# Performance work log

Hardware: AMD Instinct MI355X
Metric: run time of the kernel (lower is better)

The kernel has to match this reference:

```python
import jax, jax.numpy as jnp
import numpy as np

NPOINT = 1024   # samples (farthest point sampling count)
RADIUS = 0.2    # ball query radius
K = 32          # neighbors per ball


def farthest_point_sample(xyz, npoint):
    # xyz: [B, N, 3] -> idx: [B, npoint] int32
    B, N, _ = xyz.shape
    def body(carry, _):
        dists, farthest = carry                      # [B,N], [B]
        centroid = jnp.take_along_axis(xyz, farthest[:, None, None], axis=1)  # [B,1,3]
        d = jnp.sum((xyz - centroid) ** 2, axis=-1)  # [B,N]
        dists = jnp.minimum(dists, d)
        nxt = jnp.argmax(dists, axis=-1).astype(jnp.int32)
        return (dists, nxt), farthest
    init = (jnp.full((B, N), 1e10, dtype=xyz.dtype), jnp.zeros((B,), jnp.int32))
    _, idx = jax.lax.scan(body, init, None, length=npoint)
    return jnp.transpose(idx)  # [B, npoint]


def query_ball_point(radius, k, xyz, new_xyz):
    # returns idx: [B, S, k] int32 -- first k in-radius point indices,
    # padded with the first found index (TF query_ball_point semantics)
    N = xyz.shape[1]
    sqd = jnp.sum((new_xyz[:, :, None, :] - xyz[:, None, :, :]) ** 2, axis=-1)  # [B,S,N]
    cand = jnp.where(sqd <= radius * radius, jnp.arange(N, dtype=jnp.int32)[None, None, :], N)
    idx = jnp.sort(cand, axis=-1)[..., :k]          # [B,S,k]
    first = idx[..., :1]
    return jnp.where(idx == N, first, idx).astype(jnp.int32)


def group_point(x, idx):
    # x: [B,N,C], idx: [B,S,k] -> [B,S,k,C]
    return jax.vmap(lambda xb, ib: xb[ib])(x, idx)


def setup_inputs() -> dict:
    key = jax.random.key(0)
    ks = jax.random.split(key, 8)
    B, N, C = 16, 4096, 64
    xyz = jax.random.uniform(ks[0], (B, N, 3), dtype=jnp.float32)
    points = jax.random.normal(ks[1], (B, N, C), dtype=jnp.float32)
    cin = 3 + C  # use_xyz concat
    widths = [64, 64, 128]
    W, b, c = [], [], cin
    for i, w in enumerate(widths):
        W.append(jax.random.normal(ks[2 + i], (c, w), dtype=jnp.float32) * (1.0 / np.sqrt(c)))
        b.append(jnp.zeros((w,), dtype=jnp.float32))
        c = w
    return {"xyz": xyz, "points": points,
            "W0": W[0], "b0": b[0], "W1": W[1], "b1": b[1], "W2": W[2], "b2": b[2]}


def reference(xyz, points, W0, b0, W1, b1, W2, b2):
    # --- sample_and_group ---
    fps_idx = farthest_point_sample(xyz, NPOINT)                 # [B,S]
    new_xyz = jax.vmap(lambda xb, ib: xb[ib])(xyz, fps_idx)      # [B,S,3]
    idx = query_ball_point(RADIUS, K, xyz, new_xyz)              # [B,S,K]
    grouped_xyz = group_point(xyz, idx) - new_xyz[:, :, None, :] # [B,S,K,3]
    grouped_points = group_point(points, idx)                    # [B,S,K,C]
    new_points = jnp.concatenate([grouped_xyz, grouped_points], axis=-1)  # [B,S,K,3+C]
    # --- shared 1x1-conv MLP (bn=False, relu) ---
    for W, bb in ((W0, b0), (W1, b1), (W2, b2)):
        new_points = jax.nn.relu(jnp.einsum('bskc,cd->bskd', new_points, W) + bb)
    # --- max pool over neighborhood ---
    new_points = jnp.max(new_points, axis=2)                     # [B,S,Cout]
    return new_xyz, new_points, idx
```

## Files before the change

### kernel.cpp

```cpp
#include <hip/hip_runtime.h>

#define BB 16
#define NN 4096
#define SS 1024
#define KNB 32
#define FPT 16
#define FNW 4

typedef unsigned long long ull;
typedef float v2f __attribute__((ext_vector_type(2)));

__device__ __forceinline__ float sqd3(float dx, float dy, float dz) {
    return __fadd_rn(__fadd_rn(__fmul_rn(dx, dx), __fmul_rn(dy, dy)), __fmul_rn(dz, dz));
}

#define DPPMAX(m, ctrl, rm)                                                              \
    {                                                                                    \
        unsigned _t = (unsigned)__builtin_amdgcn_update_dpp((int)(m), (int)(m), (ctrl),  \
                                                            (rm), 0xf, false);           \
        (m) = ((m) > _t) ? (m) : _t;                                                     \
    }

__global__ __launch_bounds__(256) void fused1_kernel(const float* __restrict__ xyz,
                                                     const float* __restrict__ points,
                                                     const float* __restrict__ W0,
                                                     const float* __restrict__ b0,
                                                     float* __restrict__ P1,
                                                     float4* __restrict__ xyz4,
                                                     float* __restrict__ out_newxyz) {
    __shared__ union {
        struct {
            float4 pts4[NN];
            ull    keys[2][FNW];
            int    hist[SS];
        } f;
        float w0s[67 * 64];
    } sm;

    const int t = threadIdx.x;

    if (blockIdx.x < BB) {
        const int b = blockIdx.x;
        const int lane = t & 63;
        const float* src = xyz + (size_t)b * (NN * 3) + (size_t)t * (FPT * 3);

        v2f px2[8], py2[8], pz2[8], d2[8];
        {
            float c48[48];
#pragma unroll
            for (int m = 0; m < 12; ++m) {
                float4 v = ((const float4*)src)[m];
                c48[4 * m + 0] = v.x; c48[4 * m + 1] = v.y;
                c48[4 * m + 2] = v.z; c48[4 * m + 3] = v.w;
            }
#pragma unroll
            for (int j = 0; j < 8; ++j) {
                px2[j] = (v2f){c48[6 * j + 0], c48[6 * j + 3]};
                py2[j] = (v2f){c48[6 * j + 1], c48[6 * j + 4]};
                pz2[j] = (v2f){c48[6 * j + 2], c48[6 * j + 5]};
                d2[j]  = (v2f){1e10f, 1e10f};
                sm.f.pts4[t * FPT + 2 * j + 0] = make_float4(px2[j].x, py2[j].x, pz2[j].x, 0.f);
                sm.f.pts4[t * FPT + 2 * j + 1] = make_float4(px2[j].y, py2[j].y, pz2[j].y, 0.f);
            }
        }
        __syncthreads();

        int far = 0;
        for (int it = 0; it < SS; ++it) {
            if (t == 0) sm.f.hist[it] = far;
            if (it == SS - 1) break;
            float4 c = sm.f.pts4[far];

            float bv0 = -1.f, bv1 = -1.f;
            int bn0 = 0, bn1 = 0;
            {
#pragma clang fp contract(off)
                v2f cx2 = {c.x, c.x}, cy2 = {c.y, c.y}, cz2 = {c.z, c.z};
#pragma unroll
                for (int j = 0; j < 4; ++j) {
                    v2f dx = px2[j] - cx2;
                    v2f dy = py2[j] - cy2;
                    v2f dz = pz2[j] - cz2;
                    v2f s = (dx * dx + dy * dy) + dz * dz;
                    float d0 = fminf(d2[j].x, s.x);
                    float d1 = fminf(d2[j].y, s.y);
                    d2[j] = (v2f){d0, d1};
                    bool g0 = d0 > bv0; bv0 = g0 ? d0 : bv0; bn0 = g0 ? (t * FPT + 2 * j + 0) : bn0;
                    bool g1 = d1 > bv0; bv0 = g1 ? d1 : bv0; bn0 = g1 ? (t * FPT + 2 * j + 1) : bn0;
                }
#pragma unroll
                for (int j = 4; j < 8; ++j) {
                    v2f dx = px2[j] - cx2;
                    v2f dy = py2[j] - cy2;
                    v2f dz = pz2[j] - cz2;
                    v2f s = (dx * dx + dy * dy) + dz * dz;
                    float d0 = fminf(d2[j].x, s.x);
                    float d1 = fminf(d2[j].y, s.y);
                    d2[j] = (v2f){d0, d1};
                    bool g0 = d0 > bv1; bv1 = g0 ? d0 : bv1; bn1 = g0 ? (t * FPT + 2 * j + 0) : bn1;
                    bool g1 = d1 > bv1; bv1 = g1 ? d1 : bv1; bn1 = g1 ? (t * FPT + 2 * j + 1) : bn1;
                }
            }
            bool gm = bv1 > bv0;
            float bv = gm ? bv1 : bv0;
            int bn = gm ? bn1 : bn0;

            unsigned mb = __float_as_uint(bv);
            DPPMAX(mb, 0x111, 0xf);
            DPPMAX(mb, 0x112, 0xf);
            DPPMAX(mb, 0x114, 0xf);
            DPPMAX(mb, 0x118, 0xf);
            DPPMAX(mb, 0x142, 0xa);
            DPPMAX(mb, 0x143, 0xc);
            unsigned vmb = (unsigned)__builtin_amdgcn_readlane((int)mb, 63);

            ull ball = __ballot(__float_as_uint(bv) == vmb);
            int sel = __ffsll(ball) - 1;
            int widx = __builtin_amdgcn_readlane(bn, sel);

            const int par = it & 1;
            if (lane == 0) {
                sm.f.keys[par][t >> 6] = ((ull)vmb << 32) | (unsigned)(~widx);
            }
            __syncthreads();
            ulonglong2 ka = *(const ulonglong2*)&sm.f.keys[par][0];
            ulonglong2 kb = *(const ulonglong2*)&sm.f.keys[par][2];
            ull a0 = (ka.x > ka.y) ? ka.x : ka.y;
            ull a1 = (kb.x > kb.y) ? kb.x : kb.y;
            ull best = (a0 > a1) ? a0 : a1;
            far = (int)(~(unsigned)best);
        }
        __syncthreads();
#pragma unroll
        for (int r = 0; r < 4; ++r) {
            int it2 = t + 256 * r;
            int fi = sm.f.hist[it2];
            float4 c = sm.f.pts4[fi];
            size_t o = ((size_t)b * SS + it2) * 3;
            out_newxyz[o + 0] = c.x;
            out_newxyz[o + 1] = c.y;
            out_newxyz[o + 2] = c.z;
        }
    } else {
        for (int i = t; i < 67 * 64; i += 256) sm.w0s[i] = W0[i];
        __syncthreads();
        const int lane = t & 63;
        const int wv = t >> 6;

        {
            int n0 = (blockIdx.x - BB) * 256 + t;
            xyz4[n0] = make_float4(xyz[3 * n0 + 0], xyz[3 * n0 + 1], xyz[3 * n0 + 2], 0.f);
        }

        const float bias = b0[lane];
        const int base = (blockIdx.x - BB) * 256 + wv * 64;
        for (int pi = 0; pi < 64; ++pi) {
            const int n = base + pi;
            const float* xp = xyz + (size_t)n * 3;
            const float* pp = points + (size_t)n * 64;
            float acc = bias;
            acc = fmaf(xp[0], sm.w0s[0 * 64 + lane], acc);
            acc = fmaf(xp[1], sm.w0s[1 * 64 + lane], acc);
            acc = fmaf(xp[2], sm.w0s[2 * 64 + lane], acc);
#pragma unroll 8
            for (int c = 0; c < 64; ++c) acc = fmaf(pp[c], sm.w0s[(3 + c) * 64 + lane], acc);
            P1[(size_t)n * 64 + lane] = acc;
        }
    }
}

__global__ __launch_bounds__(256, 2) void k3_kernel(const float4* __restrict__ xyz4,
                                                    const float* __restrict__ P1,
                                                    const float* __restrict__ W0,
                                                    const float* __restrict__ W1,
                                                    const float* __restrict__ b1,
                                                    const float* __restrict__ W2,
                                                    const float* __restrict__ b2,
                                                    float* __restrict__ d_out) {
    const int t = threadIdx.x;
    const int lane = t & 63;
    const int wv = t >> 6;
    const int b = blockIdx.x >> 10;

    __shared__ float w2t[128][68];
    __shared__ float hs[4][8][64];
    __shared__ float part[4][128];
    __shared__ int   ids[KNB];
    __shared__ int   bq[2][FNW];

    float* out_newxyz = d_out;
    float* out_points = d_out + (size_t)BB * SS * 3;
    float* out_idx    = d_out + (size_t)BB * SS * 3 + (size_t)BB * SS * 128;

    const size_t q = (size_t)blockIdx.x;
    const float nx = out_newxyz[q * 3 + 0];
    const float ny = out_newxyz[q * 3 + 1];
    const float nz = out_newxyz[q * 3 + 2];

#pragma unroll
    for (int r = 0; r < 8; ++r) {
        int m = t + 256 * r;
        int o = m & 127;
        int i4 = m >> 7;
        float4 v;
        v.x = W2[(4 * i4 + 0) * 128 + o];
        v.y = W2[(4 * i4 + 1) * 128 + o];
        v.z = W2[(4 * i4 + 2) * 128 + o];
        v.w = W2[(4 * i4 + 3) * 128 + o];
        *(float4*)&w2t[o][4 * i4] = v;
    }

    {
        const float4* xb4 = xyz4 + (size_t)b * NN;
        const float R2 = 0.04f;
        const ull ltm = (1ull << lane) - 1ull;
        int total = 0, c0 = 0, pr = 0;
        float4 pcA = xb4[t];
        float4 pcB = xb4[256 + t];
        while (true) {
            float4 curA = pcA, curB = pcB;
            int nc0 = c0 + 512;
            if (nc0 < NN) {
                pcA = xb4[nc0 + t];
                pcB = xb4[nc0 + 256 + t];
            }
            float dA = sqd3(curA.x - nx, curA.y - ny, curA.z - nz);
            float dB = sqd3(curB.x - nx, curB.y - ny, curB.z - nz);
            bool inA = (dA <= R2);
            bool inB = (dB <= R2);
            ull mA = __ballot(inA);
            ull mB = __ballot(inB);
            if (lane == 0) bq[pr][wv] = __popcll(mA) | (__popcll(mB) << 8);
            __syncthreads();
            int p0 = bq[pr][0], p1 = bq[pr][1], p2 = bq[pr][2], p3 = bq[pr][3];
            int a0 = p0 & 0xff, a1 = p1 & 0xff, a2 = p2 & 0xff, a3 = p3 & 0xff;
            int e0 = p0 >> 8, e1 = p1 >> 8, e2 = p2 >> 8, e3 = p3 >> 8;
            int sumA = a0 + a1 + a2 + a3;
            int baseA = total + (wv > 0 ? a0 : 0) + (wv > 1 ? a1 : 0) + (wv > 2 ? a2 : 0);
            int baseB = total + sumA + (wv > 0 ? e0 : 0) + (wv > 1 ? e1 : 0) + (wv > 2 ? e2 : 0);
            int posA = baseA + __popcll(mA & ltm);
            int posB = baseB + __popcll(mB & ltm);
            if (inA && posA < KNB) ids[posA] = c0 + t;
            if (inB && posB < KNB) ids[posB] = c0 + 256 + t;
            total += sumA + e0 + e1 + e2 + e3;
            c0 = nc0;
            pr ^= 1;
            if (total >= KNB || c0 >= NN) break;
        }
        __syncthreads();
        int cnt = (total < KNB) ? total : KNB;
        if (t >= cnt && t < KNB) ids[t] = ids[0];
    }
    __syncthreads();
    if (t < KNB) out_idx[q * KNB + t] = (float)ids[t];

    const float qv = nx * W0[lane] + ny * W0[64 + lane] + nz * W0[128 + lane];
    float w1col[64];
#pragma unroll
    for (int i = 0; i < 64; ++i) w1col[i] = W1[i * 64 + lane];
    const float b1v = b1[lane];

    const float* P1b = P1 + (size_t)b * NN * 64;
#pragma unroll
    for (int kk = 0; kk < 8; ++kk) {
        int n = ids[wv * 8 + kk];
        float v = P1b[(size_t)n * 64 + lane] - qv;
        hs[wv][kk][lane] = fmaxf(v, 0.f);
    }

    float acc[8];
#pragma unroll
    for (int kk = 0; kk < 8; ++kk) acc[kk] = b1v;
#pragma unroll
    for (int qd = 0; qd < 16; ++qd) {
#pragma unroll
        for (int kk = 0; kk < 8; ++kk) {
            float4 h4 = *(const float4*)&hs[wv][kk][4 * qd];
            acc[kk] = fmaf(h4.x, w1col[4 * qd + 0], acc[kk]);
            acc[kk] = fmaf(h4.y, w1col[4 * qd + 1], acc[kk]);
            acc[kk] = fmaf(h4.z, w1col[4 * qd + 2], acc[kk]);
            acc[kk] = fmaf(h4.w, w1col[4 * qd + 3], acc[kk]);
        }
    }
#pragma unroll
    for (int kk = 0; kk < 8; ++kk) hs[wv][kk][lane] = fmaxf(acc[kk], 0.f);

    const float b2a = b2[lane];
    const float b2bv = b2[64 + lane];
    float acc3a[8], acc3b[8];
#pragma unroll
    for (int kk = 0; kk < 8; ++kk) { acc3a[kk] = b2a; acc3b[kk] = b2bv; }
#pragma unroll
    for (int qd = 0; qd < 16; ++qd) {
        float4 wa = *(const float4*)&w2t[lane][4 * qd];
        float4 wb = *(const float4*)&w2t[64 + lane][4 * qd];
#pragma unroll
        for (int kk = 0; kk < 8; ++kk) {
            float4 h4 = *(const float4*)&hs[wv][kk][4 * qd];
            acc3a[kk] = fmaf(h4.x, wa.x, acc3a[kk]);
            acc3a[kk] = fmaf(h4.y, wa.y, acc3a[kk]);
            acc3a[kk] = fmaf(h4.z, wa.z, acc3a[kk]);
            acc3a[kk] = fmaf(h4.w, wa.w, acc3a[kk]);
            acc3b[kk] = fmaf(h4.x, wb.x, acc3b[kk]);
            acc3b[kk] = fmaf(h4.y, wb.y, acc3b[kk]);
            acc3b[kk] = fmaf(h4.z, wb.z, acc3b[kk]);
            acc3b[kk] = fmaf(h4.w, wb.w, acc3b[kk]);
        }
    }
    float ma = 0.f, mbv = 0.f;
#pragma unroll
    for (int kk = 0; kk < 8; ++kk) {
        ma = fmaxf(ma, acc3a[kk]);
        mbv = fmaxf(mbv, acc3b[kk]);
    }
    part[wv][lane] = ma;
    part[wv][64 + lane] = mbv;
    __syncthreads();
    if (t < 128) {
        float v = fmaxf(fmaxf(part[0][t], part[1][t]), fmaxf(part[2][t], part[3][t]));
        out_points[q * 128 + t] = v;
    }
}

extern "C" void kernel_launch(void* const* d_in, const int* in_sizes, int n_in,
                              void* d_out, int out_size, void* d_ws, size_t ws_size,
                              hipStream_t stream) {
    const float* xyz    = (const float*)d_in[0];
    const float* points = (const float*)d_in[1];
    const float* W0     = (const float*)d_in[2];
    const float* b0     = (const float*)d_in[3];
    const float* W1     = (const float*)d_in[4];
    const float* b1     = (const float*)d_in[5];
    const float* W2     = (const float*)d_in[6];
    const float* b2     = (const float*)d_in[7];
    float* out = (float*)d_out;
    float*  P1   = (float*)d_ws;
    float4* xyz4 = (float4*)((char*)d_ws + (size_t)BB * NN * 64 * 4);

    hipLaunchKernelGGL(fused1_kernel, dim3(BB + (BB * NN) / 256), dim3(256), 0, stream,
                       xyz, points, W0, b0, P1, xyz4, out);
    hipLaunchKernelGGL(k3_kernel, dim3(BB * SS), dim3(256), 0, stream,
                       xyz4, P1, W0, W1, b1, W2, b2, out);
}
```

Before: 762.0 us.

## Replace FPS barrier with tagged spin-wait and pack two queries per k3 block

In the farthest-point-sampling loop, the per-iteration __syncthreads is replaced by a tagged volatile key exchange: each wave writes its key with an iteration tag in the low bits and spins until all four keys carry the current tag. The point index is packed into 24 bits to make room for the tag. This removes a full block barrier from the serial 1024-iteration critical path, at the cost of busy-polling LDS and relying on wave forward progress. Separately, the MLP kernel now processes two queries per 512-thread block and shares the W2 transpose staging between them, with a ball-query loop that continues until both queries finish.

After: 937.9 us. 1.23x slower.

```diff
diff --git a/kernel.cpp b/kernel.cpp
--- a/kernel.cpp
+++ b/kernel.cpp
@@ -42,7 +42,10 @@
     if (blockIdx.x < BB) {
         const int b = blockIdx.x;
         const int lane = t & 63;
+        const int wv_ = t >> 6;
         const float* src = xyz + (size_t)b * (NN * 3) + (size_t)t * (FPT * 3);
+
+        if (t < 8) ((ull*)sm.f.keys)[t] = 0ull;
 
         v2f px2[8], py2[8], pz2[8], d2[8];
         {
@@ -119,16 +122,23 @@
             int widx = __builtin_amdgcn_readlane(bn, sel);
 
             const int par = it & 1;
+            const unsigned tg = (((unsigned)it) & 0xFFu) ^ 0xA5u;
             if (lane == 0) {
-                sm.f.keys[par][t >> 6] = ((ull)vmb << 32) | (unsigned)(~widx);
-            }
-            __syncthreads();
-            ulonglong2 ka = *(const ulonglong2*)&sm.f.keys[par][0];
-            ulonglong2 kb = *(const ulonglong2*)&sm.f.keys[par][2];
-            ull a0 = (ka.x > ka.y) ? ka.x : ka.y;
-            ull a1 = (kb.x > kb.y) ? kb.x : kb.y;
+                *(volatile ull*)&sm.f.keys[par][wv_] =
+                    ((ull)vmb << 32) | ((ull)((~(unsigned)widx) & 0xFFFFFFu) << 8) | (ull)tg;
+            }
+            ull k0, k1, k2, k3;
+            {
+                volatile ull* kp = (volatile ull*)&sm.f.keys[par][0];
+                do {
+                    k0 = kp[0]; k1 = kp[1]; k2 = kp[2]; k3 = kp[3];
+                } while (((((unsigned)k0 ^ tg) | ((unsigned)k1 ^ tg) |
+                           ((unsigned)k2 ^ tg) | ((unsigned)k3 ^ tg)) & 0xFFu) != 0u);
+            }
+            ull a0 = (k0 > k1) ? k0 : k1;
+            ull a1 = (k2 > k3) ? k2 : k3;
             ull best = (a0 > a1) ? a0 : a1;
-            far = (int)(~(unsigned)best);
+            far = (int)((~(unsigned)(best >> 8)) & (NN - 1));
         }
         __syncthreads();
 #pragma unroll
@@ -169,7 +179,7 @@
     }
 }
 
-__global__ __launch_bounds__(256, 2) void k3_kernel(const float4* __restrict__ xyz4,
+__global__ __launch_bounds__(512, 4) void k3_kernel(const float4* __restrict__ xyz4,
                                                     const float* __restrict__ P1,
                                                     const float* __restrict__ W0,
                                                     const float* __restrict__ W1,
@@ -180,26 +190,29 @@
     const int t = threadIdx.x;
     const int lane = t & 63;
     const int wv = t >> 6;
-    const int b = blockIdx.x >> 10;
+    const int grp = wv >> 2;
+    const int gwv = wv & 3;
+    const int ltid = (gwv << 6) | lane;
 
     __shared__ float w2t[128][68];
-    __shared__ float hs[4][8][64];
-    __shared__ float part[4][128];
-    __shared__ int   ids[KNB];
-    __shared__ int   bq[2][FNW];
+    __shared__ float hs[8][8][64];
+    __shared__ float part[8][128];
+    __shared__ int   ids[2][KNB];
+    __shared__ int   bq[2][2][FNW];
 
     float* out_newxyz = d_out;
     float* out_points = d_out + (size_t)BB * SS * 3;
     float* out_idx    = d_out + (size_t)BB * SS * 3 + (size_t)BB * SS * 128;
 
-    const size_t q = (size_t)blockIdx.x;
+    const size_t q = 2 * (size_t)blockIdx.x + grp;
+    const int b = (int)(q >> 10);
     const float nx = out_newxyz[q * 3 + 0];
     const float ny = out_newxyz[q * 3 + 1];
     const float nz = out_newxyz[q * 3 + 2];
 
 #pragma unroll
-    for (int r = 0; r < 8; ++r) {
-        int m = t + 256 * r;
+    for (int r = 0; r < 4; ++r) {
+        int m = t + 512 * r;
         int o = m & 127;
         int i4 = m >> 7;
         float4 v;
@@ -210,49 +223,43 @@
         *(float4*)&w2t[o][4 * i4] = v;
     }
 
+    int total = 0;
     {
         const float4* xb4 = xyz4 + (size_t)b * NN;
         const float R2 = 0.04f;
         const ull ltm = (1ull << lane) - 1ull;
-        int total = 0, c0 = 0, pr = 0;
-        float4 pcA = xb4[t];
-        float4 pcB = xb4[256 + t];
+        int c0 = 0, pr = 0, totalO = 0;
+        float4 pc = xb4[ltid];
         while (true) {
-            float4 curA = pcA, curB = pcB;
-            int nc0 = c0 + 512;
-            if (nc0 < NN) {
-                pcA = xb4[nc0 + t];
-                pcB = xb4[nc0 + 256 + t];
-            }
-            float dA = sqd3(curA.x - nx, curA.y - ny, curA.z - nz);
-            float dB = sqd3(curB.x - nx, curB.y - ny, curB.z - nz);
-            bool inA = (dA <= R2);
-            bool inB = (dB <= R2);
-            ull mA = __ballot(inA);
-            ull mB = __ballot(inB);
-            if (lane == 0) bq[pr][wv] = __popcll(mA) | (__popcll(mB) << 8);
+            float4 cur = pc;
+            int nc0 = c0 + 256;
+            if (nc0 < NN) pc = xb4[nc0 + ltid];
+            float d = sqd3(cur.x - nx, cur.y - ny, cur.z - nz);
+            bool in = (d <= R2);
+            ull m = __ballot(in);
+            if (lane == 0) bq[pr][grp][gwv] = __popcll(m);
             __syncthreads();
-            int p0 = bq[pr][0], p1 = bq[pr][1], p2 = bq[pr][2], p3 = bq[pr][3];
-            int a0 = p0 & 0xff, a1 = p1 & 0xff, a2 = p2 & 0xff, a3 = p3 & 0xff;
-            int e0 = p0 >> 8, e1 = p1 >> 8, e2 = p2 >> 8, e3 = p3 >> 8;
-            int sumA = a0 + a1 + a2 + a3;
-            int baseA = total + (wv > 0 ? a0 : 0) + (wv > 1 ? a1 : 0) + (wv > 2 ? a2 : 0);
-            int baseB = total + sumA + (wv > 0 ? e0 : 0) + (wv > 1 ? e1 : 0) + (wv > 2 ? e2 : 0);
-            int posA = baseA + __popcll(mA & ltm);
-            int posB = baseB + __popcll(mB & ltm);
-            if (inA && posA < KNB) ids[posA] = c0 + t;
-            if (inB && posB < KNB) ids[posB] = c0 + 256 + t;
-            total += sumA + e0 + e1 + e2 + e3;
+            int s0 = bq[pr][grp][0], s1 = bq[pr][grp][1];
+            int s2 = bq[pr][grp][2], s3 = bq[pr][grp][3];
+            int o0 = bq[pr][grp ^ 1][0], o1 = bq[pr][grp ^ 1][1];
+            int o2 = bq[pr][grp ^ 1][2], o3 = bq[pr][grp ^ 1][3];
+            int base = total + (gwv > 0 ? s0 : 0) + (gwv > 1 ? s1 : 0) + (gwv > 2 ? s2 : 0);
+            int pos = base + __popcll(m & ltm);
+            if (in && pos < KNB) ids[grp][pos] = c0 + ltid;
+            total  += s0 + s1 + s2 + s3;
+            totalO += o0 + o1 + o2 + o3;
             c0 = nc0;
             pr ^= 1;
-            if (total >= KNB || c0 >= NN) break;
+            bool doneM = (total >= KNB) || (c0 >= NN);
+            bool doneO = (totalO >= KNB) || (c0 >= NN);
+            if (doneM && doneO) break;
         }
         __syncthreads();
         int cnt = (total < KNB) ? total : KNB;
-        if (t >= cnt && t < KNB) ids[t] = ids[0];
+        if (ltid >= cnt && ltid < KNB) ids[grp][ltid] = ids[grp][0];
     }
     __syncthreads();
-    if (t < KNB) out_idx[q * KNB + t] = (float)ids[t];
+    if (ltid < KNB) out_idx[q * KNB + ltid] = (float)ids[grp][ltid];
 
     const float qv = nx * W0[lane] + ny * W0[64 + lane] + nz * W0[128 + lane];
     float w1col[64];
@@ -263,7 +270,7 @@
     const float* P1b = P1 + (size_t)b * NN * 64;
 #pragma unroll
     for (int kk = 0; kk < 8; ++kk) {
-        int n = ids[wv * 8 + kk];
+        int n = ids[grp][gwv * 8 + kk];
         float v = P1b[(size_t)n * 64 + lane] - qv;
         hs[wv][kk][lane] = fmaxf(v, 0.f);
     }
@@ -316,9 +323,12 @@
     part[wv][lane] = ma;
     part[wv][64 + lane] = mbv;
     __syncthreads();
-    if (t < 128) {
-        float v = fmaxf(fmaxf(part[0][t], part[1][t]), fmaxf(part[2][t], part[3][t]));
-        out_points[q * 128 + t] = v;
+    if (t < 256) {
+        int g = t >> 7;
+        int ch = t & 127;
+        float v = fmaxf(fmaxf(part[4 * g + 0][ch], part[4 * g + 1][ch]),
+                        fmaxf(part[4 * g + 2][ch], part[4 * g + 3][ch]));
+        out_points[(2 * (size_t)blockIdx.x + g) * 128 + ch] = v;
     }
 }
 
@@ -339,6 +349,6 @@
 
     hipLaunchKernelGGL(fused1_kernel, dim3(BB + (BB * NN) / 256), dim3(256), 0, stream,
                        xyz, points, W0, b0, P1, xyz4, out);
-    hipLaunchKernelGGL(k3_kernel, dim3(BB * SS), dim3(256), 0, stream,
+    hipLaunchKernelGGL(k3_kernel, dim3(BB * SS / 2), dim3(512), 0, stream,
                        xyz4, P1, W0, W1, b1, W2, b2, out);
 }
```
